# Performance work log

Measured on AMD Instinct MI355X. Metric: run time of the kernel, lower is better.

Reference implementation:

```python
import jax, jax.numpy as jnp
import numpy as np

D_MODEL = 768
D_STATE = 128
D_CONV = 4
EXPAND = 4
D_INNER = EXPAND * D_MODEL  # 3072
DT_RANK = 48  # ceil(768/16), mamba default dt_rank='auto'
H_MLP = 768
EPS = 1e-6


def setup_inputs() -> dict:
    key = jax.random.key(0)
    ks = jax.random.split(key, 12)
    B, T = 1, 384

    def rn(k, shape, s=0.02):
        return jax.random.normal(k, shape, jnp.float32) * s

    inp = {}
    inp["x"] = jax.random.normal(ks[0], (B, 3 * T, D_MODEL), jnp.float32)
    inp["ln_w"] = jnp.ones((6, D_MODEL), jnp.float32)  # ln1..ln6 RMSNorm weights
    # 3 independent Mamba blocks, params stacked on leading dim
    inp["in_proj_w"] = rn(ks[1], (3, 2 * D_INNER, D_MODEL))
    inp["conv_w"] = rn(ks[2], (3, D_INNER, 1, D_CONV), 0.1)  # depthwise causal conv1d
    inp["conv_b"] = rn(ks[3], (3, D_INNER), 0.1)
    inp["x_proj_w"] = rn(ks[4], (3, DT_RANK + 2 * D_STATE, D_INNER))
    inp["dt_proj_w"] = rn(ks[5], (3, D_INNER, DT_RANK), 0.1)
    inp["dt_proj_b"] = rn(ks[6], (3, D_INNER), 0.1) - 4.0  # small dt after softplus
    A = jnp.tile(jnp.arange(1, D_STATE + 1, dtype=jnp.float32)[None, None, :], (3, D_INNER, 1))
    inp["A_log"] = jnp.log(A)  # mamba S4D-real init
    inp["D_skip"] = jnp.ones((3, D_INNER), jnp.float32)
    inp["out_proj_w"] = rn(ks[7], (3, D_MODEL, D_INNER))
    # 3 GatedMLPs: fc1 -> 2*hidden (value, gate), silu gate, fc2 -> out
    inp["fc1_w"] = rn(ks[8], (3, 2 * H_MLP, D_MODEL))
    inp["fc1_b"] = jnp.zeros((3, 2 * H_MLP), jnp.float32)
    inp["fc2_w"] = rn(ks[9], (3, D_MODEL, H_MLP))
    inp["fc2_b"] = jnp.zeros((3, D_MODEL), jnp.float32)
    return inp


def _rmsnorm(x, w):
    v = jnp.mean(jnp.square(x), axis=-1, keepdims=True)
    return x * jax.lax.rsqrt(v + EPS) * w


def _mamba(u, in_w, cw, cb, xp_w, dt_w, dt_b, A_log, D_skip, out_w):
    # u: (B, T, D_MODEL)
    Bsz = u.shape[0]
    xz = u @ in_w.T  # (B,T,2*Di)
    x, z = jnp.split(xz, 2, axis=-1)
    # causal depthwise conv1d over time
    xc = jax.lax.conv_general_dilated(
        jnp.swapaxes(x, 1, 2), cw, (1,), [(D_CONV - 1, 0)],
        feature_group_count=D_INNER)  # (B,Di,T)
    x = jax.nn.silu(jnp.swapaxes(xc, 1, 2) + cb)  # (B,T,Di)
    x_dbl = x @ xp_w.T  # (B,T,dt_rank+2N)
    dt = x_dbl[..., :DT_RANK]
    Bm = x_dbl[..., DT_RANK:DT_RANK + D_STATE]
    Cm = x_dbl[..., DT_RANK + D_STATE:]
    delta = jax.nn.softplus(dt @ dt_w.T + dt_b)  # (B,T,Di)
    A = -jnp.exp(A_log)  # (Di,N)

    def step(h, inp):
        d_t, B_t, C_t, u_t = inp  # (B,Di),(B,N),(B,N),(B,Di)
        h = jnp.exp(d_t[:, :, None] * A) * h + (d_t * u_t)[:, :, None] * B_t[:, None, :]
        y = jnp.einsum('bdn,bn->bd', h, C_t)
        return h, y

    h0 = jnp.zeros((Bsz, D_INNER, D_STATE), u.dtype)
    xs = tuple(jnp.swapaxes(a, 0, 1) for a in (delta, Bm, Cm, x))  # time-major
    _, ys = jax.lax.scan(jax.checkpoint(step), h0, xs)
    y = jnp.swapaxes(ys, 0, 1) + x * D_skip  # (B,T,Di)
    return (y * jax.nn.silu(z)) @ out_w.T  # (B,T,D_MODEL)


def _gmlp(x, w1, b1, w2, b2):
    h = x @ w1.T + b1
    a, g = jnp.split(h, 2, axis=-1)
    return (jax.nn.silu(g) * a) @ w2.T + b2


def reference(x, ln_w, in_proj_w, conv_w, conv_b, x_proj_w, dt_proj_w, dt_proj_b,
              A_log, D_skip, out_proj_w, fc1_w, fc1_b, fc2_w, fc2_b):
    t = x.shape[1] // 3
    outs = []
    for i in range(3):  # music / up / down branches
        b = x[:, i * t:(i + 1) * t]
        b = b + _mamba(_rmsnorm(b, ln_w[2 * i]), in_proj_w[i], conv_w[i], conv_b[i],
                       x_proj_w[i], dt_proj_w[i], dt_proj_b[i], A_log[i], D_skip[i],
                       out_proj_w[i])
        b = b + _gmlp(_rmsnorm(b, ln_w[2 * i + 1]), fc1_w[i], fc1_b[i], fc2_w[i], fc2_b[i])
        outs.append(b)
    return jnp.concatenate(outs, axis=1)
```

## Files before the change

### kernel.cpp

```cpp
#include <hip/hip_runtime.h>
#include <hip/hip_bf16.h>

#define TSEQ 384
#define DMODEL 768
#define DINNER 3072
#define DSTATE 128
#define DTRANK 48
#define XPROJ_N (DTRANK + 2*DSTATE)
#define NSEG 3
#define LOG2E 1.44269504088896340736f
#define LN2F  0.69314718055994530942f

typedef __attribute__((ext_vector_type(8))) short short8;
typedef __attribute__((ext_vector_type(4))) float floatx4;
typedef unsigned short u16;
typedef unsigned int u32;

__device__ __forceinline__ float bf2f(u16 u) {
    return __uint_as_float(((unsigned)u) << 16);
}
__device__ __forceinline__ float ldf(const void* p, size_t i, int bf) {
    return bf ? bf2f(((const u16*)p)[i]) : ((const float*)p)[i];
}
__device__ __forceinline__ void stf(void* p, size_t i, float v, int bf) {
    if (bf) ((__hip_bfloat16*)p)[i] = __float2bfloat16(v);
    else    ((float*)p)[i] = v;
}
__device__ __forceinline__ float silu_f(float v) { return v / (1.f + __expf(-v)); }
__device__ __forceinline__ u16 f2bf(float f) {
    unsigned u = __float_as_uint(f);
    return (u16)((u + 0x7FFFu + ((u >> 16) & 1u)) >> 16);
}

__device__ __forceinline__ float exp2_fast(float x) {
#if __has_builtin(__builtin_amdgcn_exp2f)
    return __builtin_amdgcn_exp2f(x);
#else
    return exp2f(x);
#endif
}

template<int CTRL>
__device__ __forceinline__ float ror_add(float x) {
    int r = __builtin_amdgcn_update_dpp(0, __float_as_int(x), CTRL, 0xF, 0xF, true);
    return x + __int_as_float(r);
}

__device__ __forceinline__ void gl16(const void* g, void* l) {
    __builtin_amdgcn_global_load_lds(
        (const __attribute__((address_space(1))) u32*)g,
        (__attribute__((address_space(3))) u32*)l, 16, 0, 0);
}

__global__ void k_detect(const unsigned* lnw_bits, int* flag) {
    if (threadIdx.x == 0) {
        flag[0] = (lnw_bits[0] == 0x3F803F80u) ? 1 : 0;
    }
}

__global__ __launch_bounds__(256) void k_rmsnorm(
    const void* src, int src_is_f32, const void* lnw, int wbase,
    u16* out, const int* flagp)
{
    int bf  = *flagp;
    int sbf = src_is_f32 ? 0 : bf;
    int r   = blockIdx.x;
    int seg = r / TSEQ;
    int wrow = 2*seg + wbase;
    int tid = threadIdx.x;
    float v[3]; float s = 0.f;
    #pragma unroll
    for (int j = 0; j < 3; ++j) {
        int e = j*256 + tid;
        v[j] = ldf(src, (size_t)r*DMODEL + e, sbf);
        s += v[j]*v[j];
    }
    __shared__ float red[256];
    red[tid] = s; __syncthreads();
    for (int st = 128; st > 0; st >>= 1) {
        if (tid < st) red[tid] += red[tid+st];
        __syncthreads();
    }
    float rs = rsqrtf(red[0]/(float)DMODEL + 1e-6f);
    #pragma unroll
    for (int j = 0; j < 3; ++j) {
        int e = j*256 + tid;
        out[(size_t)r*DMODEL + e] = f2bf(v[j]*rs*ldf(lnw, (size_t)wrow*DMODEL + e, bf));
    }
}

__global__ __launch_bounds__(256) void k_gemm(
    const float* A, const void* W, const void* bias,
    float* C, const int* flagp, int M, int N, int K, int lda)
{
    int bf  = *flagp;
    int seg = blockIdx.z;
    int mbase = blockIdx.y * 64, nbase = blockIdx.x * 64;
    int tid = threadIdx.x;
    int tx = tid & 15, ty = tid >> 4;

    __shared__ float As[16][68];
    __shared__ float Ws[16][68];

    const float* Ag = A + (size_t)seg*M*lda;
    size_t segW = (size_t)seg*N*K;

    int lrow = tid >> 2;
    int lk   = (tid & 3) * 4;
    int wn   = nbase + lrow;

    float acc[4][4];
    #pragma unroll
    for (int i = 0; i < 4; ++i)
        #pragma unroll
        for (int j = 0; j < 4; ++j) acc[i][j] = 0.f;

    for (int kt = 0; kt < K; kt += 16) {
        float4 av = *reinterpret_cast<const float4*>(Ag + (size_t)(mbase+lrow)*lda + kt + lk);
        As[lk+0][lrow] = av.x; As[lk+1][lrow] = av.y;
        As[lk+2][lrow] = av.z; As[lk+3][lrow] = av.w;
        float w0=0.f, w1=0.f, w2=0.f, w3=0.f;
        if (wn < N) {
            size_t off = segW + (size_t)wn*K + kt + lk;
            if (bf) {
                ushort4 q = *reinterpret_cast<const ushort4*>((const u16*)W + off);
                w0 = bf2f(q.x); w1 = bf2f(q.y); w2 = bf2f(q.z); w3 = bf2f(q.w);
            } else {
                float4 f = *reinterpret_cast<const float4*>((const float*)W + off);
                w0 = f.x; w1 = f.y; w2 = f.z; w3 = f.w;
            }
        }
        Ws[lk+0][lrow] = w0; Ws[lk+1][lrow] = w1;
        Ws[lk+2][lrow] = w2; Ws[lk+3][lrow] = w3;
        __syncthreads();
        #pragma unroll
        for (int kk = 0; kk < 16; ++kk) {
            float4 a4 = *reinterpret_cast<const float4*>(&As[kk][ty*4]);
            float4 b4 = *reinterpret_cast<const float4*>(&Ws[kk][tx*4]);
            float ar[4] = {a4.x, a4.y, a4.z, a4.w};
            float br[4] = {b4.x, b4.y, b4.z, b4.w};
            #pragma unroll
            for (int i = 0; i < 4; ++i)
                #pragma unroll
                for (int j = 0; j < 4; ++j)
                    acc[i][j] = fmaf(ar[i], br[j], acc[i][j]);
        }
        __syncthreads();
    }

    #pragma unroll
    for (int i = 0; i < 4; ++i) {
        int m = mbase + ty*4 + i;
        #pragma unroll
        for (int j = 0; j < 4; ++j) {
            int n = nbase + tx*4 + j;
            if (n < N) {
                float v = acc[i][j] + ldf(bias, (size_t)seg*N + n, bf);
                v = (v > 20.f) ? v : log1pf(__expf(v));
                C[((size_t)(seg*M + m))*N + n] = v;
            }
        }
    }
}

#define LP2 72
__global__ __launch_bounds__(256) void k_gemm_mfma64(
    const u16* A, const void* W, const void* bias, const void* resid,
    int resid_flagged, void* C, int c_mode, const int* flagp,
    int M, int N, int K)
{
    int bf  = *flagp;
    int seg = blockIdx.z;
    int mbase = blockIdx.y * 64, nbase = blockIdx.x * 64;
    int tid = threadIdx.x;
    int w = tid >> 6, lane = tid & 63;
    int wm = w >> 1, wn = w & 1;
    int quad = lane >> 4, l16 = lane & 15;

    __shared__ short As[64 * LP2];
    __shared__ short Ws[64 * LP2];

    const u16* Ag = A + (size_t)seg*M*K + (size_t)mbase*K;
    size_t segW = (size_t)seg*N*K;

    int sr  = tid >> 2;
    int skc = (tid & 3) * 16;

    floatx4 acc[2][2];
    #pragma unroll
    for (int i = 0; i < 2; ++i)
        #pragma unroll
        for (int j = 0; j < 2; ++j)
            acc[i][j] = (floatx4){0.f, 0.f, 0.f, 0.f};

    int wrow = nbase + sr;
    for (int kt = 0; kt < K; kt += 64) {
        const u16* ap = Ag + (size_t)sr*K + kt + skc;
        *reinterpret_cast<short8*>(&As[sr*LP2 + skc])     = *reinterpret_cast<const short8*>(ap);
        *reinterpret_cast<short8*>(&As[sr*LP2 + skc + 8]) = *reinterpret_cast<const short8*>(ap + 8);
        {
            short8 s0 = (short8){0,0,0,0,0,0,0,0}, s1 = s0;
            if (wrow < N) {
                size_t off = segW + (size_t)wrow*K + kt + skc;
                if (bf) {
                    s0 = *reinterpret_cast<const short8*>((const u16*)W + off);
                    s1 = *reinterpret_cast<const short8*>((const u16*)W + off + 8);
                } else {
                    const float* wp = (const float*)W + off;
                    float f[16];
                    #pragma unroll
                    for (int q = 0; q < 4; ++q) {
                        float4 v = *reinterpret_cast<const float4*>(wp + q*4);
                        f[q*4+0] = v.x; f[q*4+1] = v.y; f[q*4+2] = v.z; f[q*4+3] = v.w;
                    }
                    #pragma unroll
                    for (int q = 0; q < 8; ++q) { s0[q] = (short)f2bf(f[q]); s1[q] = (short)f2bf(f[q+8]); }
                }
            }
            *reinterpret_cast<short8*>(&Ws[sr*LP2 + skc])     = s0;
            *reinterpret_cast<short8*>(&Ws[sr*LP2 + skc + 8]) = s1;
        }
        __syncthreads();
        #pragma unroll
        for (int kk = 0; kk < 2; ++kk) {
            short8 af[2], bfr[2];
            #pragma unroll
            for (int i = 0; i < 2; ++i)
                af[i] = *reinterpret_cast<const short8*>(&As[(wm*32 + i*16 + l16)*LP2 + kk*32 + quad*8]);
            #pragma unroll
            for (int j = 0; j < 2; ++j)
                bfr[j] = *reinterpret_cast<const short8*>(&Ws[(wn*32 + j*16 + l16)*LP2 + kk*32 + quad*8]);
            #pragma unroll
            for (int i = 0; i < 2; ++i)
                #pragma unroll
                for (int j = 0; j < 2; ++j)
                    acc[i][j] = __builtin_amdgcn_mfma_f32_16x16x32_bf16(af[i], bfr[j], acc[i][j], 0, 0, 0);
        }
        __syncthreads();
    }

    #pragma unroll
    for (int i = 0; i < 2; ++i) {
        #pragma unroll
        for (int reg = 0; reg < 4; ++reg) {
            int grow = mbase + wm*32 + i*16 + quad*4 + reg;
            #pragma unroll
            for (int j = 0; j < 2; ++j) {
                int gcol = nbase + wn*32 + j*16 + l16;
                if (gcol < N) {
                    float v = acc[i][j][reg];
                    if (bias) v += ldf(bias, (size_t)seg*N + gcol, bf);
                    size_t idx = ((size_t)(seg*M + grow))*N + gcol;
                    if (resid) v += resid_flagged ? ldf(resid, idx, bf)
                                                  : ((const float*)resid)[idx];
                    if      (c_mode == 0) ((float*)C)[idx] = v;
                    else if (c_mode == 1) ((u16*)C)[idx] = f2bf(v);
                    else                  stf(C, idx, v, bf);
                }
            }
        }
    }
}

__global__ __launch_bounds__(256) void k_gemm_mfma64g(
    const u16* A, const void* W, const void* bias, const void* resid,
    int resid_flagged, void* C, int c_mode, const int* flagp,
    int M, int N, int K)
{
    int bf  = *flagp;
    int seg = blockIdx.z;
    int mbase = blockIdx.y * 64, nbase = blockIdx.x * 64;
    int tid = threadIdx.x;
    int w = tid >> 6, lane = tid & 63;
    int wm = w >> 1, wn = w & 1;
    int quad = lane >> 4, l16 = lane & 15;

    __shared__ short As[3][64*64];
    __shared__ short Ws[3][64*64];

    const u16* Ag  = A + (size_t)seg*M*K + (size_t)mbase*K;
    const u16* Wgp = (const u16*)W + (size_t)seg*N*K + (size_t)nbase*K;
    int nk = K >> 6;

    int srow = lane >> 3;
    int scol = ((lane & 7) ^ srow) * 8;
    int swz  = (l16 & 7) * 8;

    floatx4 acc[2][2];
    #pragma unroll
    for (int i = 0; i < 2; ++i)
        #pragma unroll
        for (int j = 0; j < 2; ++j)
            acc[i][j] = (floatx4){0.f, 0.f, 0.f, 0.f};

    auto CMP = [&](int b) {
        #pragma unroll
        for (int kk = 0; kk < 2; ++kk) {
            short8 af[2], bfr[2];
            #pragma unroll
            for (int i = 0; i < 2; ++i) {
                int row = wm*32 + i*16 + l16;
                af[i] = *reinterpret_cast<const short8*>(
                    &As[b][row*64 + (((kk*4 + quad)*8) ^ swz)]);
            }
            #pragma unroll
            for (int j = 0; j < 2; ++j) {
                int row = wn*32 + j*16 + l16;
                bfr[j] = *reinterpret_cast<const short8*>(
                    &Ws[b][row*64 + (((kk*4 + quad)*8) ^ swz)]);
            }
            #pragma unroll
            for (int i = 0; i < 2; ++i)
                #pragma unroll
                for (int j = 0; j < 2; ++j)
                    acc[i][j] = __builtin_amdgcn_mfma_f32_16x16x32_bf16(af[i], bfr[j], acc[i][j], 0, 0, 0);
        }
    };

    if (bf) {
        auto STG = [&](int t, int b) {
            size_t kt = (size_t)t << 6;
            #pragma unroll
            for (int i8 = 0; i8 < 2; ++i8) {
                int rbase = w*16 + i8*8;
                gl16(Ag  + (size_t)(rbase + srow)*K + kt + scol, &As[b][rbase*64]);
                gl16(Wgp + (size_t)(rbase + srow)*K + kt + scol, &Ws[b][rbase*64]);
            }
        };
        STG(0, 0);
        STG(1, 1);
        for (int t = 0; t < nk - 2; ++t) {
            STG(t + 2, (t + 2) % 3);
            asm volatile("s_waitcnt vmcnt(8)" ::: "memory");
            __builtin_amdgcn_s_barrier();
            __builtin_amdgcn_sched_barrier(0);
            CMP(t % 3);
            asm volatile("" ::: "memory");
            __builtin_amdgcn_s_barrier();
        }
        asm volatile("s_waitcnt vmcnt(4)" ::: "memory");
        __builtin_amdgcn_s_barrier();
        __builtin_amdgcn_sched_barrier(0);
        CMP((nk - 2) % 3);
        asm volatile("" ::: "memory");
        __builtin_amdgcn_s_barrier();
        asm volatile("s_waitcnt vmcnt(0)" ::: "memory");
        __builtin_amdgcn_s_barrier();
        __builtin_amdgcn_sched_barrier(0);
        CMP((nk - 1) % 3);
    } else {
        const float* Wf = (const float*)W + (size_t)seg*N*K + (size_t)nbase*K;
        int row2 = tid >> 2;
        for (int t = 0; t < nk; ++t) {
            size_t kt = (size_t)t << 6;
            #pragma unroll
            for (int i8 = 0; i8 < 2; ++i8) {
                int rbase = w*16 + i8*8;
                gl16(Ag + (size_t)(rbase + srow)*K + kt + scol, &As[0][rbase*64]);
            }
            const float* wp = Wf + (size_t)row2*K + kt;
            #pragma unroll
            for (int h2 = 0; h2 < 2; ++h2) {
                int gs = (tid & 3) + h2*4;
                short8 s;
                #pragma unroll
                for (int q2 = 0; q2 < 8; ++q2) s[q2] = (short)f2bf(wp[gs*8 + q2]);
                *reinterpret_cast<short8*>(&Ws[0][row2*64 + ((gs ^ (row2 & 7)) * 8)]) = s;
            }
            __syncthreads();
            CMP(0);
            __syncthreads();
        }
    }

    #pragma unroll
    for (int i = 0; i < 2; ++i) {
        #pragma unroll
        for (int reg = 0; reg < 4; ++reg) {
            int grow = mbase + wm*32 + i*16 + quad*4 + reg;
            #pragma unroll
            for (int j = 0; j < 2; ++j) {
                int gcol = nbase + wn*32 + j*16 + l16;
                float v = acc[i][j][reg];
                if (bias) v += ldf(bias, (size_t)seg*N + gcol, bf);
                size_t idx = ((size_t)(seg*M + grow))*N + gcol;
                if (resid) v += resid_flagged ? ldf(resid, idx, bf)
                                              : ((const float*)resid)[idx];
                if      (c_mode == 0) ((float*)C)[idx] = v;
                else if (c_mode == 1) ((u16*)C)[idx] = f2bf(v);
                else                  stf(C, idx, v, bf);
            }
        }
    }
}

__global__ __launch_bounds__(256) void k_fc1_gate_g(
    const u16* A, const void* W, const void* bias, u16* act, const int* flagp)
{
    const int M = TSEQ, K = DMODEL, NF = 2*DMODEL;
    int bf  = *flagp;
    int seg = blockIdx.z;
    int mbase = blockIdx.y * 64, nbase = blockIdx.x * 64;
    int tid = threadIdx.x;
    int w = tid >> 6, lane = tid & 63;
    int wm = w >> 1, wn = w & 1;
    int quad = lane >> 4, l16 = lane & 15;

    __shared__ short As[2][64*64];
    __shared__ short Wa[2][64*64];
    __shared__ short Wg[2][64*64];

    const u16* Ag  = A + (size_t)seg*M*K + (size_t)mbase*K;
    const u16* Wap = (const u16*)W + (size_t)seg*NF*K + (size_t)nbase*K;
    const u16* Wgp = Wap + (size_t)DMODEL*K;
    int nk = K >> 6;

    int srow = lane >> 3;
    int scol = ((lane & 7) ^ srow) * 8;
    int swz  = (l16 & 7) * 8;

    floatx4 acca[2][2], accg[2][2];
    #pragma unroll
    for (int i = 0; i < 2; ++i)
        #pragma unroll
        for (int j = 0; j < 2; ++j) {
            acca[i][j] = (floatx4){0.f, 0.f, 0.f, 0.f};
            accg[i][j] = (floatx4){0.f, 0.f, 0.f, 0.f};
        }

    auto CMP = [&](int b) {
        #pragma unroll
        for (int kk = 0; kk < 2; ++kk) {
            short8 af[2], ba[2], bg[2];
            #pragma unroll
            for (int i = 0; i < 2; ++i) {
                int row = wm*32 + i*16 + l16;
                af[i] = *reinterpret_cast<const short8*>(
                    &As[b][row*64 + (((kk*4 + quad)*8) ^ swz)]);
            }
            #pragma unroll
            for (int j = 0; j < 2; ++j) {
                int row = wn*32 + j*16 + l16;
                int col = ((kk*4 + quad)*8) ^ swz;
                ba[j] = *reinterpret_cast<const short8*>(&Wa[b][row*64 + col]);
                bg[j] = *reinterpret_cast<const short8*>(&Wg[b][row*64 + col]);
            }
            #pragma unroll
            for (int i = 0; i < 2; ++i)
                #pragma unroll
                for (int j = 0; j < 2; ++j) {
                    acca[i][j] = __builtin_amdgcn_mfma_f32_16x16x32_bf16(af[i], ba[j], acca[i][j], 0, 0, 0);
                    accg[i][j] = __builtin_amdgcn_mfma_f32_16x16x32_bf16(af[i], bg[j], accg[i][j], 0, 0, 0);
                }
        }
    };

    if (bf) {
        auto STG = [&](int t, int b) {
            size_t kt = (size_t)t << 6;
            #pragma unroll
            for (int i8 = 0; i8 < 2; ++i8) {
                int rbase = w*16 + i8*8;
                size_t so = (size_t)(rbase + srow)*K + kt + scol;
                gl16(Ag  + so, &As[b][rbase*64]);
                gl16(Wap + so, &Wa[b][rbase*64]);
                gl16(Wgp + so, &Wg[b][rbase*64]);
            }
        };
        STG(0, 0);
        for (int t = 0; t < nk - 1; ++t) {
            STG(t + 1, (t + 1) & 1);
            asm volatile("s_waitcnt vmcnt(6)" ::: "memory");
            __builtin_amdgcn_s_barrier();
            __builtin_amdgcn_sched_barrier(0);
            CMP(t & 1);
            asm volatile("" ::: "memory");
            __builtin_amdgcn_s_barrier();
        }
        asm volatile("s_waitcnt vmcnt(0)" ::: "memory");
        __builtin_amdgcn_s_barrier();
        __builtin_amdgcn_sched_barrier(0);
        CMP((nk - 1) & 1);
    } else {
        const float* Waf = (const float*)W + (size_t)seg*NF*K + (size_t)nbase*K;
        const float* Wgf = Waf + (size_t)DMODEL*K;
        int row2 = tid >> 2;
        for (int t = 0; t < nk; ++t) {
            size_t kt = (size_t)t << 6;
            #pragma unroll
            for (int i8 = 0; i8 < 2; ++i8) {
                int rbase = w*16 + i8*8;
                gl16(Ag + (size_t)(rbase + srow)*K + kt + scol, &As[0][rbase*64]);
            }
            #pragma unroll
            for (int h2 = 0; h2 < 2; ++h2) {
                int gs = (tid & 3) + h2*4;
                int wcol = (gs ^ (row2 & 7)) * 8;
                short8 sa, sg;
                const float* wpa = Waf + (size_t)row2*K + kt + gs*8;
                const float* wpg = Wgf + (size_t)row2*K + kt + gs*8;
                #pragma unroll
                for (int q2 = 0; q2 < 8; ++q2) { sa[q2] = (short)f2bf(wpa[q2]); sg[q2] = (short)f2bf(wpg[q2]); }
                *reinterpret_cast<short8*>(&Wa[0][row2*64 + wcol]) = sa;
                *reinterpret_cast<short8*>(&Wg[0][row2*64 + wcol]) = sg;
            }
            __syncthreads();
            CMP(0);
            __syncthreads();
        }
    }

    #pragma unroll
    for (int i = 0; i < 2; ++i) {
        #pragma unroll
        for (int reg = 0; reg < 4; ++reg) {
            int grow = mbase + wm*32 + i*16 + quad*4 + reg;
            #pragma unroll
            for (int j = 0; j < 2; ++j) {
                int gcol = nbase + wn*32 + j*16 + l16;
                float va = acca[i][j][reg] + ldf(bias, (size_t)seg*NF + gcol, bf);
                float vg = accg[i][j][reg] + ldf(bias, (size_t)seg*NF + DMODEL + gcol, bf);
                act[((size_t)(seg*M + grow))*DMODEL + gcol] = f2bf(va * silu_f(vg));
            }
        }
    }
}

__global__ __launch_bounds__(256) void k_conv(
    const u16* xz, const void* cw, const void* cb, u16* xconv, const int* flagp)
{
    int bf = *flagp;
    size_t gid = (size_t)blockIdx.x*256 + threadIdx.x;
    int d = (int)(gid % DINNER);
    size_t rt = gid / DINNER;
    int t = (int)(rt % TSEQ);
    int seg = (int)(rt / TSEQ);
    float acc = ldf(cb, (size_t)seg*DINNER + d, bf);
    const u16* xs = xz + (size_t)seg*TSEQ*(2*DINNER);
    #pragma unroll
    for (int j = 0; j < 4; ++j) {
        int ts = t - 3 + j;
        if (ts >= 0)
            acc = fmaf(ldf(cw, ((size_t)seg*DINNER + d)*4 + j, bf),
                       bf2f(xs[(size_t)ts*(2*DINNER) + d]), acc);
    }
    xconv[gid] = f2bf(silu_f(acc));
}

#define WSCH 4
#define WSCT 8
#define NPAIR (TSEQ/(2*WSCT))
#define NBX   (DINNER/WSCH)
#define GUARD_TH 0.04f

__global__ __launch_bounds__(64) void k_scan_wave(
    const float* delta, const u16* xconv, const float* xdbl, const u16* xz,
    const void* A_log, const void* D_skip, u16* yout, const int* flagp)
{
    int bf   = flagp[0];
    int seg  = blockIdx.y;
    int bx = (int)blockIdx.x;
    bx = (bx & 7) * (NBX/8) + (bx >> 3);
    int dbase = bx * WSCH;
    int lane = threadIdx.x;
    int ch = lane >> 4, sl = lane & 15;
    int d = dbase + ch;

    __shared__ float4 BUF[2][WSCT][64];
    __shared__ float  DLB2[WSCT][8];

    float a[8];
    size_t abase = ((size_t)seg*DINNER + d)*DSTATE + (size_t)sl*8;
    #pragma unroll
    for (int j = 0; j < 8; ++j)
        a[j] = -__expf(ldf(A_log, abase + j, bf)) * LOG2E;
    float gl[8]; float gmax = 0.f;
    gl[0] = 0.f;
    #pragma unroll
    for (int j = 1; j < 8; ++j) {
        gl[j] = (a[j] - a[j-1]) * LN2F;
        gmax = fmaxf(gmax, fabsf(gl[j]));
    }
    float wg = gmax;
    #pragma unroll
    for (int k = 32; k >= 1; k >>= 1) wg = fmaxf(wg, __shfl_xor(wg, k));
    float a0  = a[0];
    float Dsk = ldf(D_skip, (size_t)seg*DINNER + d, bf);
    float dskg = (sl == 0) ? Dsk : 0.f;

    const float* xdbl_s = xdbl + (size_t)seg*TSEQ*XPROJ_N;
    int loff = DTRANK + (lane & 15)*8 + ((lane >> 4) & 1)*4 + ((lane >> 5) ? DSTATE : 0);
    const float* srcl = xdbl_s + loff;

    const float* delta_s = delta + (size_t)seg*TSEQ*DINNER + dbase;
    const u16*   xconv_s = xconv + (size_t)seg*TSEQ*DINNER + dbase;
    const u16*   z_s     = xz    + (size_t)seg*TSEQ*(2*DINNER) + DINNER + dbase + ch;
    u16*         y_s     = yout  + (size_t)seg*TSEQ*DINNER + dbase + ch;

    float4  pdel = (float4){0.f, 0.f, 0.f, 0.f};
    ushort4 pu   = (ushort4){0, 0, 0, 0};
    u16     pz   = 0;

    auto STAGE = [&](int tile, int buf) {
        const float* rb = srcl + (size_t)tile*WSCT*XPROJ_N;
        #pragma unroll
        for (int t = 0; t < WSCT; ++t)
            gl16(rb + (size_t)t*XPROJ_N, &BUF[buf][t][0]);
    };
    auto PLOAD = [&](int tile) {
        if (lane < WSCT) {
            size_t ro = (size_t)(tile*WSCT + lane)*DINNER;
            pdel = *reinterpret_cast<const float4*>(delta_s + ro);
            pu   = *reinterpret_cast<const ushort4*>(xconv_s + ro);
        }
    };
    auto DSTORE = [&]() -> bool {
        if (lane < WSCT) {
            float4 w0 = (float4){pdel.x, bf2f(pu.x), pdel.y, bf2f(pu.y)};
            float4 w1 = (float4){pdel.z, bf2f(pu.z), pdel.w, bf2f(pu.w)};
            *reinterpret_cast<float4*>(&DLB2[lane][0]) = w0;
            *reinterpret_cast<float4*>(&DLB2[lane][4]) = w1;
        }
        float m4 = fmaxf(fmaxf(pdel.x, pdel.y), fmaxf(pdel.z, pdel.w));
        return __any(m4 * wg > GUARD_TH);
    };

    float h[8];
    #pragma unroll
    for (int j = 0; j < 8; ++j) h[j] = 0.f;
    float yr = 0.f;

    float2 duA, duB;
    float4 b0A, b1A, c0A, c1A;
    float4 b0B, b1B, c0B, c1B;

#define LOADOPS(BP, T, S) do {                                                \
    du##S = *reinterpret_cast<const float2*>(&DLB2[T][ch*2]);                 \
    b0##S = (BP)[(T)*64 + sl];                                                \
    b1##S = (BP)[(T)*64 + 16 + sl];                                           \
    c0##S = (BP)[(T)*64 + 32 + sl];                                           \
    c1##S = (BP)[(T)*64 + 48 + sl];                                           \
} while (0)

#define COMPUTE(S, T) do {                                                    \
    float del = du##S.x, ut = du##S.y;                                        \
    float duu = del * ut;                                                     \
    float e0,e1,e2,e3,e4,e5,e6,e7;                                            \
    if (gf) {                                                                 \
        e0 = exp2_fast(del * a0);                                             \
        e1 = e0 * fmaf(del, gl[1], 1.f);                                      \
        e2 = e1 * fmaf(del, gl[2], 1.f);                                      \
        e3 = e2 * fmaf(del, gl[3], 1.f);                                      \
        e4 = e3 * fmaf(del, gl[4], 1.f);                                      \
        e5 = e4 * fmaf(del, gl[5], 1.f);                                      \
        e6 = e5 * fmaf(del, gl[6], 1.f);                                      \
        e7 = e6 * fmaf(del, gl[7], 1.f);                                      \
    } else {                                                                  \
        e0 = exp2_fast(del*a[0]); e1 = exp2_fast(del*a[1]);                   \
        e2 = exp2_fast(del*a[2]); e3 = exp2_fast(del*a[3]);                   \
        e4 = exp2_fast(del*a[4]); e5 = exp2_fast(del*a[5]);                   \
        e6 = exp2_fast(del*a[6]); e7 = exp2_fast(del*a[7]);                   \
    }                                                                         \
    h[0] = fmaf(e0, h[0], duu*b0##S.x);                                       \
    h[1] = fmaf(e1, h[1], duu*b0##S.y);                                       \
    h[2] = fmaf(e2, h[2], duu*b0##S.z);                                       \
    h[3] = fmaf(e3, h[3], duu*b0##S.w);                                       \
    h[4] = fmaf(e4, h[4], duu*b1##S.x);                                       \
    h[5] = fmaf(e5, h[5], duu*b1##S.y);                                       \
    h[6] = fmaf(e6, h[6], duu*b1##S.z);                                       \
    h[7] = fmaf(e7, h[7], duu*b1##S.w);                                       \
    float p0 = ut * dskg;                                                     \
    p0 = fmaf(h[0], c0##S.x, p0);                                             \
    p0 = fmaf(h[1], c0##S.y, p0);                                             \
    p0 = fmaf(h[2], c0##S.z, p0);                                             \
    p0 = fmaf(h[3], c0##S.w, p0);                                             \
    float p1 = h[4]*c1##S.x;                                                  \
    p1 = fmaf(h[5], c1##S.y, p1);                                             \
    p1 = fmaf(h[6], c1##S.z, p1);                                             \
    p1 = fmaf(h[7], c1##S.w, p1);                                             \
    float p = p0 + p1;                                                        \
    p = ror_add<0x128>(p);                                                    \
    p = ror_add<0x124>(p);                                                    \
    p = ror_add<0x122>(p);                                                    \
    p = ror_add<0x121>(p);                                                    \
    if (sl == (half8 | (T))) yr = p;                                          \
} while (0)

    auto do_tile = [&](const float4* bp, bool gf, int half8) {
        LOADOPS(bp, 0, A);
        LOADOPS(bp, 1, B);
        COMPUTE(A, 0);
        LOADOPS(bp, 2, A);
        COMPUTE(B, 1);
        LOADOPS(bp, 3, B);
        COMPUTE(A, 2);
        LOADOPS(bp, 4, A);
        COMPUTE(B, 3);
        LOADOPS(bp, 5, B);
        COMPUTE(A, 4);
        LOADOPS(bp, 6, A);
        COMPUTE(B, 5);
        LOADOPS(bp, 7, B);
        COMPUTE(A, 6);
        COMPUTE(B, 7);
    };

    STAGE(0, 0);
    PLOAD(0);

    for (int p = 0; p < NPAIR; ++p) {
        int tA = 2*p;
        asm volatile("s_waitcnt vmcnt(0)" ::: "memory");
        bool exA = DSTORE();
        STAGE(tA + 1, 1);
        PLOAD(tA + 1);
        pz = z_s[(size_t)(p*16 + sl) * (size_t)(2*DINNER)];
        __builtin_amdgcn_sched_barrier(0);
        do_tile(&BUF[0][0][0], !exA, 0);
        asm volatile("s_waitcnt vmcnt(0)" ::: "memory");
        bool exB = DSTORE();
        if (tA + 2 < 2*NPAIR) {
            STAGE(tA + 2, 0);
            PLOAD(tA + 2);
        }
        __builtin_amdgcn_sched_barrier(0);
        do_tile(&BUF[1][0][0], !exB, 8);
        y_s[(size_t)(p*16 + sl) * (size_t)DINNER] = f2bf(yr * silu_f(bf2f(pz)));
        yr = 0.f;
    }
#undef LOADOPS
#undef COMPUTE
}

extern "C" void kernel_launch(void* const* d_in, const int* in_sizes, int n_in,
                              void* d_out, int out_size, void* d_ws, size_t ws_size,
                              hipStream_t stream) {
    const void* x     = d_in[0];
    const void* lnw   = d_in[1];
    const void* inw   = d_in[2];
    const void* convw = d_in[3];
    const void* convb = d_in[4];
    const void* xpw   = d_in[5];
    const void* dtw   = d_in[6];
    const void* dtb   = d_in[7];
    const void* alog  = d_in[8];
    const void* dsk   = d_in[9];
    const void* outw  = d_in[10];
    const void* fc1w  = d_in[11];
    const void* fc1b  = d_in[12];
    const void* fc2w  = d_in[13];
    const void* fc2b  = d_in[14];

    int* flag = (int*)d_ws;
    char* wsb = (char*)d_ws;
    const size_t N_U    = (size_t)NSEG*TSEQ*DMODEL;
    const size_t N_XZ   = (size_t)NSEG*TSEQ*2*DINNER;
    const size_t N_XC   = (size_t)NSEG*TSEQ*DINNER;
    const size_t N_XDBL = (size_t)NSEG*TSEQ*XPROJ_N;

    u16*   u     = (u16*)(wsb + 16);
    u16*   xz    = u + N_U;
    u16*   xconv = xz + N_XZ;
    float* xdbl  = (float*)(xconv + N_XC);
    float* delta = xdbl + N_XDBL;
    u16*   yfin  = (u16*)(delta + N_XC);
    float* b1    = (float*)(yfin + N_XC);
    u16*   actb  = (u16*)(b1 + N_U);

    k_detect<<<1, 64, 0, stream>>>((const unsigned*)lnw, flag);

    k_rmsnorm<<<NSEG*TSEQ, 256, 0, stream>>>(x, 0, lnw, 0, u, flag);
    k_gemm_mfma64g<<<dim3(96, 6, NSEG), 256, 0, stream>>>(u, inw, nullptr, nullptr, 0,
        xz, 1, flag, TSEQ, 2*DINNER, DMODEL);
    k_conv<<<(NSEG*TSEQ*DINNER)/256, 256, 0, stream>>>(xz, convw, convb, xconv, flag);
    k_gemm_mfma64<<<dim3(5, 6, NSEG), 256, 0, stream>>>(xconv, xpw, nullptr, nullptr, 0,
        xdbl, 0, flag, TSEQ, XPROJ_N, DINNER);
    k_gemm<<<dim3(48, 6, NSEG), 256, 0, stream>>>(xdbl, dtw, dtb,
        delta, flag, TSEQ, DINNER, DTRANK, XPROJ_N);

    k_scan_wave<<<dim3(NBX, NSEG), 64, 0, stream>>>(
        delta, xconv, xdbl, xz, alog, dsk, yfin, flag);

    k_gemm_mfma64g<<<dim3(12, 6, NSEG), 256, 0, stream>>>(yfin, outw, nullptr, x, 1,
        b1, 0, flag, TSEQ, DMODEL, DINNER);

    k_rmsnorm<<<NSEG*TSEQ, 256, 0, stream>>>(b1, 1, lnw, 1, u, flag);
    k_fc1_gate_g<<<dim3(12, 6, NSEG), 256, 0, stream>>>(u, fc1w, fc1b, actb, flag);
    k_gemm_mfma64g<<<dim3(12, 6, NSEG), 256, 0, stream>>>(actb, fc2w, fc2b, b1, 0,
        d_out, 2, flag, TSEQ, DMODEL, DMODEL);
}
```

Baseline: 551.0 us.

## Unify GEMMs on pipelined async-load kernel and deepen scan operand prefetch

Removes the simple synchronous LDS GEMM used for the x_proj projection and generalizes the triple-buffered async-load swizzled GEMM to handle N not divisible by 64 by clamping weight rows, so the x_proj GEMM (K=3072) gets the pipelined path. The scan kernel's per-tile loop now keeps three operand sets in flight instead of two, so loads are issued further ahead of compute. The extra operand set raises register pressure in the scan, and the clamped rows load duplicate weight data that is then discarded.

```diff
diff --git a/kernel.cpp b/kernel.cpp
--- a/kernel.cpp
+++ b/kernel.cpp
@@ -163,8 +163,7 @@
     }
 }
 
-#define LP2 72
-__global__ __launch_bounds__(256) void k_gemm_mfma64(
+__global__ __launch_bounds__(256) void k_gemm_mfma64g(
     const u16* A, const void* W, const void* bias, const void* resid,
     int resid_flagged, void* C, int c_mode, const int* flagp,
     int M, int N, int K)
@@ -177,14 +176,16 @@
     int wm = w >> 1, wn = w & 1;
     int quad = lane >> 4, l16 = lane & 15;
 
-    __shared__ short As[64 * LP2];
-    __shared__ short Ws[64 * LP2];
+    __shared__ short As[3][64*64];
+    __shared__ short Ws[3][64*64];
 
     const u16* Ag = A + (size_t)seg*M*K + (size_t)mbase*K;
-    size_t segW = (size_t)seg*N*K;
-
-    int sr  = tid >> 2;
-    int skc = (tid & 3) * 16;
+    size_t segWK = (size_t)seg*N*K;
+    int nk = K >> 6;
+
+    int srow = lane >> 3;
+    int scol = ((lane & 7) ^ srow) * 8;
+    int swz  = (l16 & 7) * 8;
 
     floatx4 acc[2][2];
     #pragma unroll
@@ -193,50 +194,88 @@
         for (int j = 0; j < 2; ++j)
             acc[i][j] = (floatx4){0.f, 0.f, 0.f, 0.f};
 
-    int wrow = nbase + sr;
-    for (int kt = 0; kt < K; kt += 64) {
-        const u16* ap = Ag + (size_t)sr*K + kt + skc;
-        *reinterpret_cast<short8*>(&As[sr*LP2 + skc])     = *reinterpret_cast<const short8*>(ap);
-        *reinterpret_cast<short8*>(&As[sr*LP2 + skc + 8]) = *reinterpret_cast<const short8*>(ap + 8);
-        {
-            short8 s0 = (short8){0,0,0,0,0,0,0,0}, s1 = s0;
-            if (wrow < N) {
-                size_t off = segW + (size_t)wrow*K + kt + skc;
-                if (bf) {
-                    s0 = *reinterpret_cast<const short8*>((const u16*)W + off);
-                    s1 = *reinterpret_cast<const short8*>((const u16*)W + off + 8);
-                } else {
-                    const float* wp = (const float*)W + off;
-                    float f[16];
-                    #pragma unroll
-                    for (int q = 0; q < 4; ++q) {
-                        float4 v = *reinterpret_cast<const float4*>(wp + q*4);
-                        f[q*4+0] = v.x; f[q*4+1] = v.y; f[q*4+2] = v.z; f[q*4+3] = v.w;
-                    }
-                    #pragma unroll
-                    for (int q = 0; q < 8; ++q) { s0[q] = (short)f2bf(f[q]); s1[q] = (short)f2bf(f[q+8]); }
-                }
-            }
-            *reinterpret_cast<short8*>(&Ws[sr*LP2 + skc])     = s0;
-            *reinterpret_cast<short8*>(&Ws[sr*LP2 + skc + 8]) = s1;
-        }
-        __syncthreads();
+    auto CMP = [&](int b) {
         #pragma unroll
         for (int kk = 0; kk < 2; ++kk) {
             short8 af[2], bfr[2];
             #pragma unroll
-            for (int i = 0; i < 2; ++i)
-                af[i] = *reinterpret_cast<const short8*>(&As[(wm*32 + i*16 + l16)*LP2 + kk*32 + quad*8]);
-            #pragma unroll
-            for (int j = 0; j < 2; ++j)
-                bfr[j] = *reinterpret_cast<const short8*>(&Ws[(wn*32 + j*16 + l16)*LP2 + kk*32 + quad*8]);
+            for (int i = 0; i < 2; ++i) {
+                int row = wm*32 + i*16 + l16;
+                af[i] = *reinterpret_cast<const short8*>(
+                    &As[b][row*64 + (((kk*4 + quad)*8) ^ swz)]);
+            }
+            #pragma unroll
+            for (int j = 0; j < 2; ++j) {
+                int row = wn*32 + j*16 + l16;
+                bfr[j] = *reinterpret_cast<const short8*>(
+                    &Ws[b][row*64 + (((kk*4 + quad)*8) ^ swz)]);
+            }
             #pragma unroll
             for (int i = 0; i < 2; ++i)
                 #pragma unroll
                 for (int j = 0; j < 2; ++j)
                     acc[i][j] = __builtin_amdgcn_mfma_f32_16x16x32_bf16(af[i], bfr[j], acc[i][j], 0, 0, 0);
         }
-        __syncthreads();
+    };
+
+    if (bf) {
+        const u16* Wb = (const u16*)W;
+        auto STG = [&](int t, int b) {
+            size_t kt = (size_t)t << 6;
+            #pragma unroll
+            for (int i8 = 0; i8 < 2; ++i8) {
+                int rbase = w*16 + i8*8;
+                gl16(Ag + (size_t)(rbase + srow)*K + kt + scol, &As[b][rbase*64]);
+                int wr = nbase + rbase + srow;
+                if (wr > N - 1) wr = N - 1;
+                gl16(Wb + segWK + (size_t)wr*K + kt + scol, &Ws[b][rbase*64]);
+            }
+        };
+        STG(0, 0);
+        STG(1, 1);
+        for (int t = 0; t < nk - 2; ++t) {
+            STG(t + 2, (t + 2) % 3);
+            asm volatile("s_waitcnt vmcnt(8)" ::: "memory");
+            __builtin_amdgcn_s_barrier();
+            __builtin_amdgcn_sched_barrier(0);
+            CMP(t % 3);
+            asm volatile("" ::: "memory");
+            __builtin_amdgcn_s_barrier();
+        }
+        asm volatile("s_waitcnt vmcnt(4)" ::: "memory");
+        __builtin_amdgcn_s_barrier();
+        __builtin_amdgcn_sched_barrier(0);
+        CMP((nk - 2) % 3);
+        asm volatile("" ::: "memory");
+        __builtin_amdgcn_s_barrier();
+        asm volatile("s_waitcnt vmcnt(0)" ::: "memory");
+        __builtin_amdgcn_s_barrier();
+        __builtin_amdgcn_sched_barrier(0);
+        CMP((nk - 1) % 3);
+    } else {
+        const float* Wf = (const float*)W + segWK;
+        int row2 = tid >> 2;
+        int wr2 = nbase + row2; if (wr2 > N - 1) wr2 = N - 1;
+        for (int t = 0; t < nk; ++t) {
+            size_t kt = (size_t)t << 6;
+            #pragma unroll
+            for (int i8 = 0; i8 < 2; ++i8) {
+                int rbase = w*16 + i8*8;
+                gl16(Ag + (size_t)(rbase + srow)*K + kt + scol, &As[0][rbase*64]);
+            }
+            const float* wp = Wf + (size_t)wr2*K + kt;
+            #pragma unroll
+            for (int h2 = 0; h2 < 2; ++h2) {
+                int gs = (tid & 3) + h2*4;
+                short8 s;
+                #pragma unroll
+                for (int q2 = 0; q2 < 8; ++q2) s[q2] = (short)f2bf(wp[gs*8 + q2]);
+                *reinterpret_cast<short8*>(&Ws[0][row2*64 + ((gs ^ (row2 & 7)) * 8)]) = s;
+            }
+            __syncthreads();
+            CMP(0);
+            __syncthreads();
+        }
     }
 
     #pragma unroll
@@ -262,138 +301,6 @@
     }
 }
 
-__global__ __launch_bounds__(256) void k_gemm_mfma64g(
-    const u16* A, const void* W, const void* bias, const void* resid,
-    int resid_flagged, void* C, int c_mode, const int* flagp,
-    int M, int N, int K)
-{
-    int bf  = *flagp;
-    int seg = blockIdx.z;
-    int mbase = blockIdx.y * 64, nbase = blockIdx.x * 64;
-    int tid = threadIdx.x;
-    int w = tid >> 6, lane = tid & 63;
-    int wm = w >> 1, wn = w & 1;
-    int quad = lane >> 4, l16 = lane & 15;
-
-    __shared__ short As[3][64*64];
-    __shared__ short Ws[3][64*64];
-
-    const u16* Ag  = A + (size_t)seg*M*K + (size_t)mbase*K;
-    const u16* Wgp = (const u16*)W + (size_t)seg*N*K + (size_t)nbase*K;
-    int nk = K >> 6;
-
-    int srow = lane >> 3;
-    int scol = ((lane & 7) ^ srow) * 8;
-    int swz  = (l16 & 7) * 8;
-
-    floatx4 acc[2][2];
-    #pragma unroll
-    for (int i = 0; i < 2; ++i)
-        #pragma unroll
-        for (int j = 0; j < 2; ++j)
-            acc[i][j] = (floatx4){0.f, 0.f, 0.f, 0.f};
-
-    auto CMP = [&](int b) {
-        #pragma unroll
-        for (int kk = 0; kk < 2; ++kk) {
-            short8 af[2], bfr[2];
-            #pragma unroll
-            for (int i = 0; i < 2; ++i) {
-                int row = wm*32 + i*16 + l16;
-                af[i] = *reinterpret_cast<const short8*>(
-                    &As[b][row*64 + (((kk*4 + quad)*8) ^ swz)]);
-            }
-            #pragma unroll
-            for (int j = 0; j < 2; ++j) {
-                int row = wn*32 + j*16 + l16;
-                bfr[j] = *reinterpret_cast<const short8*>(
-                    &Ws[b][row*64 + (((kk*4 + quad)*8) ^ swz)]);
-            }
-            #pragma unroll
-            for (int i = 0; i < 2; ++i)
-                #pragma unroll
-                for (int j = 0; j < 2; ++j)
-                    acc[i][j] = __builtin_amdgcn_mfma_f32_16x16x32_bf16(af[i], bfr[j], acc[i][j], 0, 0, 0);
-        }
-    };
-
-    if (bf) {
-        auto STG = [&](int t, int b) {
-            size_t kt = (size_t)t << 6;
-            #pragma unroll
-            for (int i8 = 0; i8 < 2; ++i8) {
-                int rbase = w*16 + i8*8;
-                gl16(Ag  + (size_t)(rbase + srow)*K + kt + scol, &As[b][rbase*64]);
-                gl16(Wgp + (size_t)(rbase + srow)*K + kt + scol, &Ws[b][rbase*64]);
-            }
-        };
-        STG(0, 0);
-        STG(1, 1);
-        for (int t = 0; t < nk - 2; ++t) {
-            STG(t + 2, (t + 2) % 3);
-            asm volatile("s_waitcnt vmcnt(8)" ::: "memory");
-            __builtin_amdgcn_s_barrier();
-            __builtin_amdgcn_sched_barrier(0);
-            CMP(t % 3);
-            asm volatile("" ::: "memory");
-            __builtin_amdgcn_s_barrier();
-        }
-        asm volatile("s_waitcnt vmcnt(4)" ::: "memory");
-        __builtin_amdgcn_s_barrier();
-        __builtin_amdgcn_sched_barrier(0);
-        CMP((nk - 2) % 3);
-        asm volatile("" ::: "memory");
-        __builtin_amdgcn_s_barrier();
-        asm volatile("s_waitcnt vmcnt(0)" ::: "memory");
-        __builtin_amdgcn_s_barrier();
-        __builtin_amdgcn_sched_barrier(0);
-        CMP((nk - 1) % 3);
-    } else {
-        const float* Wf = (const float*)W + (size_t)seg*N*K + (size_t)nbase*K;
-        int row2 = tid >> 2;
-        for (int t = 0; t < nk; ++t) {
-            size_t kt = (size_t)t << 6;
-            #pragma unroll
-            for (int i8 = 0; i8 < 2; ++i8) {
-                int rbase = w*16 + i8*8;
-                gl16(Ag + (size_t)(rbase + srow)*K + kt + scol, &As[0][rbase*64]);
-            }
-            const float* wp = Wf + (size_t)row2*K + kt;
-            #pragma unroll
-            for (int h2 = 0; h2 < 2; ++h2) {
-                int gs = (tid & 3) + h2*4;
-                short8 s;
-                #pragma unroll
-                for (int q2 = 0; q2 < 8; ++q2) s[q2] = (short)f2bf(wp[gs*8 + q2]);
-                *reinterpret_cast<short8*>(&Ws[0][row2*64 + ((gs ^ (row2 & 7)) * 8)]) = s;
-            }
-            __syncthreads();
-            CMP(0);
-            __syncthreads();
-        }
-    }
-
-    #pragma unroll
-    for (int i = 0; i < 2; ++i) {
-        #pragma unroll
-        for (int reg = 0; reg < 4; ++reg) {
-            int grow = mbase + wm*32 + i*16 + quad*4 + reg;
-            #pragma unroll
-            for (int j = 0; j < 2; ++j) {
-                int gcol = nbase + wn*32 + j*16 + l16;
-                float v = acc[i][j][reg];
-                if (bias) v += ldf(bias, (size_t)seg*N + gcol, bf);
-                size_t idx = ((size_t)(seg*M + grow))*N + gcol;
-                if (resid) v += resid_flagged ? ldf(resid, idx, bf)
-                                              : ((const float*)resid)[idx];
-                if      (c_mode == 0) ((float*)C)[idx] = v;
-                else if (c_mode == 1) ((u16*)C)[idx] = f2bf(v);
-                else                  stf(C, idx, v, bf);
-            }
-        }
-    }
-}
-
 __global__ __launch_bounds__(256) void k_fc1_gate_g(
     const u16* A, const void* W, const void* bias, u16* act, const int* flagp)
 {
@@ -630,9 +537,10 @@
     for (int j = 0; j < 8; ++j) h[j] = 0.f;
     float yr = 0.f;
 
-    float2 duA, duB;
+    float2 duA, duB, duC;
     float4 b0A, b1A, c0A, c1A;
     float4 b0B, b1B, c0B, c1B;
+    float4 b0C, b1C, c0C, c1C;
 
 #define LOADOPS(BP, T, S) do {                                                \
     du##S = *reinterpret_cast<const float2*>(&DLB2[T][ch*2]);                 \
@@ -689,18 +597,18 @@
     auto do_tile = [&](const float4* bp, bool gf, int half8) {
         LOADOPS(bp, 0, A);
         LOADOPS(bp, 1, B);
+        LOADOPS(bp, 2, C);
         COMPUTE(A, 0);
-        LOADOPS(bp, 2, A);
+        LOADOPS(bp, 3, A);
         COMPUTE(B, 1);
-        LOADOPS(bp, 3, B);
-        COMPUTE(A, 2);
-        LOADOPS(bp, 4, A);
-        COMPUTE(B, 3);
-        LOADOPS(bp, 5, B);
-        COMPUTE(A, 4);
+        LOADOPS(bp, 4, B);
+        COMPUTE(C, 2);
+        LOADOPS(bp, 5, C);
+        COMPUTE(A, 3);
         LOADOPS(bp, 6, A);
-        COMPUTE(B, 5);
+        COMPUTE(B, 4);
         LOADOPS(bp, 7, B);
+        COMPUTE(C, 5);
         COMPUTE(A, 6);
         COMPUTE(B, 7);
     };
@@ -773,7 +681,7 @@
     k_gemm_mfma64g<<<dim3(96, 6, NSEG), 256, 0, stream>>>(u, inw, nullptr, nullptr, 0,
         xz, 1, flag, TSEQ, 2*DINNER, DMODEL);
     k_conv<<<(NSEG*TSEQ*DINNER)/256, 256, 0, stream>>>(xz, convw, convb, xconv, flag);
-    k_gemm_mfma64<<<dim3(5, 6, NSEG), 256, 0, stream>>>(xconv, xpw, nullptr, nullptr, 0,
+    k_gemm_mfma64g<<<dim3(5, 6, NSEG), 256, 0, stream>>>(xconv, xpw, nullptr, nullptr, 0,
         xdbl, 0, flag, TSEQ, XPROJ_N, DINNER);
     k_gemm<<<dim3(48, 6, NSEG), 256, 0, stream>>>(xdbl, dtw, dtb,
         delta, flag, TSEQ, DINNER, DTRANK, XPROJ_N);
```

Result: faster. 540.1 us (-2.0%).
